# Performance work log

Hardware: AMD Instinct MI355X
Metric: run time of the kernel (lower is better)

## Reference

```python
import jax, jax.numpy as jnp
import numpy as np


def _deform_conv2d(x, offset, weight, stride=(1, 1), pad=(1, 1), dilation=(1, 1)):
    # x: [B,C,H,W]; offset: [B, 2*Goff*kh*kw, oh, ow]; weight: [OC, C//Gw, kh, kw]
    B, C, H, W = x.shape
    OC, Cg, kh, kw = weight.shape
    Gw = C // Cg
    K = kh * kw
    sh, sw = stride
    ph, pw = pad
    dh, dw = dilation
    oh = (H + 2 * ph - (dh * (kh - 1) + 1)) // sh + 1
    ow = (W + 2 * pw - (dw * (kw - 1) + 1)) // sw + 1
    Goff = offset.shape[1] // (2 * K)
    # torchvision layout: per offset group, per kernel tap k, (dy, dx)
    off = offset.reshape(B, Goff, K, 2, oh, ow)
    ki = jnp.arange(K) // kw  # kernel row per tap
    kj = jnp.arange(K) % kw   # kernel col per tap
    base_y = jnp.arange(oh) * sh - ph
    base_x = jnp.arange(ow) * sw - pw
    gy = (base_y[None, :] + (ki * dh)[:, None]).astype(x.dtype)  # [K, oh]
    gx = (base_x[None, :] + (kj * dw)[:, None]).astype(x.dtype)  # [K, ow]
    py = off[:, :, :, 0] + gy[None, None, :, :, None]  # [B,Goff,K,oh,ow]
    px = off[:, :, :, 1] + gx[None, None, :, None, :]
    cpg = C // Goff  # channels per offset group
    py = jnp.repeat(py, cpg, axis=1)  # [B,C,K,oh,ow]
    px = jnp.repeat(px, cpg, axis=1)
    xf = x.reshape(B, C, H * W)
    y0 = jnp.floor(py)
    x0 = jnp.floor(px)
    ty = py - y0
    tx = px - x0
    y0i = y0.astype(jnp.int32)
    x0i = x0.astype(jnp.int32)

    def gather(cy, cx):
        valid = (cy >= 0) & (cy < H) & (cx >= 0) & (cx < W)
        idx = jnp.clip(cy, 0, H - 1) * W + jnp.clip(cx, 0, W - 1)
        v = jnp.take_along_axis(xf, idx.reshape(B, C, -1), axis=2).reshape(idx.shape)
        return jnp.where(valid, v, jnp.zeros((), x.dtype))

    # bilinear sample, zero padding outside image (matches torchvision)
    v = (gather(y0i, x0i) * (1 - ty) * (1 - tx)
         + gather(y0i, x0i + 1) * (1 - ty) * tx
         + gather(y0i + 1, x0i) * ty * (1 - tx)
         + gather(y0i + 1, x0i + 1) * ty * tx)  # [B,C,K,oh,ow]
    v = v.reshape(B, Gw, Cg, K, oh, ow)
    wg = weight.reshape(Gw, OC // Gw, Cg, K)
    out = jnp.einsum('bgckhw,gock->bgohw', v, wg)
    return out.reshape(B, OC, oh, ow)


def setup_inputs() -> dict:
    key = jax.random.key(0)
    k1, k2, k3 = jax.random.split(key, 3)
    x = jax.random.normal(k1, (8, 64, 56, 56), dtype=jnp.float32)
    offset = jax.random.normal(k2, (8, 18, 56, 56), dtype=jnp.float32)
    weight = jax.random.normal(k3, (64, 64, 3, 3), dtype=jnp.float32) * 0.05
    return {"input": x, "offset": offset, "weight": weight}


def reference(input, offset, weight):
    return _deform_conv2d(input, offset, weight, stride=(1, 1), pad=(1, 1), dilation=(1, 1))
```

## Files before the change

### kernel.cpp

```cpp
#include <hip/hip_runtime.h>
#include <hip/hip_fp16.h>


typedef _Float16 f16x8 __attribute__((ext_vector_type(8)));
typedef float    f32x4 __attribute__((ext_vector_type(4)));

namespace {
constexpr int Bn = 8, Cn = 64, Hn = 56, Wn = 56;
constexpr int Kk = 9, OCn = 64;
constexpr int NPIX = 56 * 56;
constexpr int CK   = Cn * Kk;
constexpr int TP   = 32;
constexpr int TILES = NPIX / TP;
constexpr int XTILES = NPIX / 64;
constexpr int KSTEPS = CK / 32;
}

__device__ __forceinline__ __half2 u2h(unsigned u) {
    union { unsigned u; __half2 h; } x; x.u = u; return x.h;
}
__device__ __forceinline__ unsigned bcast_h(float f) {
    unsigned short hs = __half_as_ushort(__float2half(f));
    return (unsigned)hs * 0x10001u;
}
__device__ __forceinline__ void lds_barrier() {
    asm volatile("s_waitcnt lgkmcnt(0)" ::: "memory");
    __builtin_amdgcn_s_barrier();
}
__device__ __forceinline__ void gld16(uint4& d, const unsigned short* p) {
    asm volatile("global_load_dwordx4 %0, %1, off" : "=&v"(d) : "v"(p) : "memory");
}

__global__ __launch_bounds__(256) void prep_kernel(
    const float* __restrict__ x, const float* __restrict__ w,
    unsigned short* __restrict__ xh, unsigned short* __restrict__ wh2)
{
    const int tid = threadIdx.x;
    if (blockIdx.x >= 392) {
        const int i = (blockIdx.x - 392) * 256 + tid;
        if (i < OCn * CK) {
            const int j    = i & 7;
            const int lane = (i >> 3) & 63;
            const int rest = i >> 9;
            const int og   = rest / KSTEPS;
            const int oc   = og * 16 + (lane & 15);
            const int kglob = (rest % KSTEPS) * 32 + (lane >> 4) * 8 + j;
            const int tap = kglob >> 6;
            const int c   = kglob & 63;
            wh2[i] = __half_as_ushort(__float2half(w[oc * CK + c * Kk + tap]));
        }
        return;
    }
    __shared__ unsigned short lds[64][66];
    const int b  = blockIdx.x / XTILES;
    const int t0 = (blockIdx.x % XTILES) * 64;
    const float* xb = x + (size_t)b * Cn * NPIX;
    {
        const int hw0 = (tid & 15) * 4;
        #pragma unroll
        for (int i = 0; i < 4; ++i) {
            const int c = (tid >> 4) + i * 16;
            const float4 v = *(const float4*)(xb + (size_t)c * NPIX + t0 + hw0);
            lds[hw0 + 0][c] = __half_as_ushort(__float2half(v.x));
            lds[hw0 + 1][c] = __half_as_ushort(__float2half(v.y));
            lds[hw0 + 2][c] = __half_as_ushort(__float2half(v.z));
            lds[hw0 + 3][c] = __half_as_ushort(__float2half(v.w));
        }
    }
    __syncthreads();
    {
        const int co = (tid & 7) * 8;
        #pragma unroll
        for (int i = 0; i < 2; ++i) {
            const int hw = (tid >> 3) + i * 32;
            unsigned short tmp[8] __attribute__((aligned(16)));
            #pragma unroll
            for (int j = 0; j < 8; ++j) tmp[j] = lds[hw][co + j];
            *(uint4*)(xh + ((size_t)b * NPIX + t0 + hw) * Cn + co) = *(const uint4*)tmp;
        }
    }
}

__global__ __launch_bounds__(256, 3) void deform_fused(
    const unsigned short* __restrict__ xh, const float* __restrict__ off,
    const unsigned short* __restrict__ wh2, float* __restrict__ out)
{
    __shared__ uint4 smpw[Kk * TP];
    __shared__ int4  smpa[Kk * TP];
    __shared__ __align__(16) uint4 vbuf[3][8 * TP];

    const int tid = threadIdx.x;
    const int b  = blockIdx.x / TILES;
    const int p0 = (blockIdx.x % TILES) * TP;
    const unsigned short* xb = xh + (size_t)b * NPIX * Cn;
    const float* offb = off + (size_t)b * 18 * NPIX;

    for (int e = tid; e < Kk * TP; e += 256) {
        const int k  = e >> 5;
        const int px = e & 31;
        const int p  = p0 + px;
        const int oy = p / Wn, ox = p % Wn;
        const int ki = k / 3, kj = k % 3;
        const float offy = offb[(size_t)(2 * k)     * NPIX + p];
        const float offx = offb[(size_t)(2 * k + 1) * NPIX + p];
        const float py  = offy + (float)(oy - 1 + ki);
        const float pxv = offx + (float)(ox - 1 + kj);
        const float y0f = floorf(py), x0f = floorf(pxv);
        const float ty = py - y0f, tx = pxv - x0f;
        const int y0 = (int)y0f, x0 = (int)x0f;
        const int y1 = y0 + 1, x1 = x0 + 1;
        const bool vy0 = (y0 >= 0) & (y0 < Hn);
        const bool vy1 = (y1 >= 0) & (y1 < Hn);
        const bool vx0 = (x0 >= 0) & (x0 < Wn);
        const bool vx1 = (x1 >= 0) & (x1 < Wn);
        const int cy0 = min(max(y0, 0), Hn - 1);
        const int cy1 = min(max(y1, 0), Hn - 1);
        const int cx0 = min(max(x0, 0), Wn - 1);
        const int cx1 = min(max(x1, 0), Wn - 1);
        uint4 wq;
        wq.x = bcast_h((vy0 && vx0) ? (1.f - ty) * (1.f - tx) : 0.f);
        wq.y = bcast_h((vy0 && vx1) ? (1.f - ty) * tx         : 0.f);
        wq.z = bcast_h((vy1 && vx0) ? ty * (1.f - tx)         : 0.f);
        wq.w = bcast_h((vy1 && vx1) ? ty * tx                 : 0.f);
        int4 av;
        av.x = (cy0 * Wn + cx0) * Cn;
        av.y = (cy0 * Wn + cx1) * Cn;
        av.z = (cy1 * Wn + cx0) * Cn;
        av.w = (cy1 * Wn + cx1) * Cn;
        smpw[e] = wq;
        smpa[e] = av;
    }
    lds_barrier();
    asm volatile("s_waitcnt vmcnt(0)" ::: "memory");

    const int oct = tid & 7;
    const int gpx = (tid >> 3) & 31;
    const int co  = oct * 8;

    const int lane = tid & 63;
    const int og   = tid >> 6;
    const int hi   = lane >> 4;
    const int lr   = lane & 15;
    const uint4* ab = (const uint4*)wh2 + (size_t)og * KSTEPS * 64 + lane;

    uint4 s0[2], s1[2], s2[2], s3[2], wqr[2];
    uint4 aF[2][2];
    f32x4 acc0 = {0.f, 0.f, 0.f, 0.f};
    f32x4 acc1 = {0.f, 0.f, 0.f, 0.f};

    auto stageC = [&](int k) {
        const int sl = k & 1;
        const int m  = k * TP + gpx;
        const int4 av = smpa[m];
        wqr[sl] = smpw[m];
        gld16(s0[sl], xb + av.x + co);
        gld16(s1[sl], xb + av.y + co);
        gld16(s2[sl], xb + av.z + co);
        gld16(s3[sl], xb + av.w + co);
    };
    auto loadA = [&](int k) {
        const int sl = k & 1;
        gld16(aF[sl][0], (const unsigned short*)(ab + (k * 2 + 0) * 64));
        gld16(aF[sl][1], (const unsigned short*)(ab + (k * 2 + 1) * 64));
    };
    auto blend = [&](int k) {
        const int sl = k & 1;
        const __half2 w00 = u2h(wqr[sl].x), w01 = u2h(wqr[sl].y);
        const __half2 w10 = u2h(wqr[sl].z), w11 = u2h(wqr[sl].w);
        uint4 res;
        unsigned* rp = (unsigned*)&res;
        #pragma unroll
        for (int q = 0; q < 4; ++q) {
            __half2 a = __hmul2(w00, u2h(((const unsigned*)&s0[sl])[q]));
            a = __hfma2(w01, u2h(((const unsigned*)&s1[sl])[q]), a);
            a = __hfma2(w10, u2h(((const unsigned*)&s2[sl])[q]), a);
            a = __hfma2(w11, u2h(((const unsigned*)&s3[sl])[q]), a);
            rp[q] = *(const unsigned*)&a;
        }
        vbuf[k % 3][oct * TP + gpx] = res;
    };
    auto mfma = [&](int k) {
        const int sl = k % 3;
        #pragma unroll
        for (int kl = 0; kl < 2; ++kl) {
            const int octr = kl * 4 + hi;
            union { uint4 u; f16x8 h; } a, b0, b1;
            a.u  = aF[k & 1][kl];
            b0.u = vbuf[sl][octr * TP + lr];
            b1.u = vbuf[sl][octr * TP + 16 + lr];
            acc0 = __builtin_amdgcn_mfma_f32_16x16x32_f16(a.h, b0.h, acc0, 0, 0, 0);
            acc1 = __builtin_amdgcn_mfma_f32_16x16x32_f16(a.h, b1.h, acc1, 0, 0, 0);
        }
    };

    stageC(0); stageC(1);
    loadA(0);
    asm volatile("s_waitcnt vmcnt(6)" ::: "memory");
    __builtin_amdgcn_sched_barrier(0);
    blend(0);
    lds_barrier();

    #pragma unroll
    for (int k = 0; k < Kk; ++k) {
        if (k < Kk - 2) stageC(k + 2);
        if (k < Kk - 1) loadA(k + 1);
        if (k < Kk - 2)      asm volatile("s_waitcnt vmcnt(6)" ::: "memory");
        else if (k == Kk - 2) asm volatile("s_waitcnt vmcnt(2)" ::: "memory");
        else                  asm volatile("s_waitcnt vmcnt(0)" ::: "memory");
        __builtin_amdgcn_sched_barrier(0);
        if (k < Kk - 1) blend(k + 1);
        mfma(k);
        lds_barrier();
    }

    float* ob = out + ((size_t)b * OCn + og * 16 + hi * 4) * NPIX + p0 + lr;
    #pragma unroll
    for (int r = 0; r < 4; ++r) {
        ob[(size_t)r * NPIX]      = acc0[r];
        ob[(size_t)r * NPIX + 16] = acc1[r];
    }
}

extern "C" void kernel_launch(void* const* d_in, const int* in_sizes, int n_in,
                              void* d_out, int out_size, void* d_ws, size_t ws_size,
                              hipStream_t stream) {
    const float* x   = (const float*)d_in[0];
    const float* off = (const float*)d_in[1];
    const float* w   = (const float*)d_in[2];
    float* out = (float*)d_out;
    unsigned short* wh2 = (unsigned short*)d_ws;
    unsigned short* xh  = (unsigned short*)((char*)d_ws + 131072);

    hipLaunchKernelGGL(prep_kernel, dim3(392 + 144), dim3(256), 0, stream, x, w, xh, wh2);
    hipLaunchKernelGGL(deform_fused, dim3(Bn * TILES), dim3(256), 0, stream,
                       xh, off, wh2, out);
}
```

Before: 22.00 us.

## Halve block size so each wave computes two output-channel groups

The fused deform conv kernel now runs 128 threads per block instead of 256. Each thread gathers and blends two pixels per tap, and each wave issues MFMAs for two 16-channel output groups, reusing the same B fragments from LDS. This cuts the thread count and the LDS reads per MFMA and gives each wave more independent MFMA work. The cost is more registers per thread, deeper vmcnt waits and fewer waves per block to hide gather latency.

Result: no change. 22.18 us (+0.8%).

```diff
diff --git a/kernel.cpp b/kernel.cpp
--- a/kernel.cpp
+++ b/kernel.cpp
@@ -81,7 +81,7 @@
     }
 }
 
-__global__ __launch_bounds__(256, 3) void deform_fused(
+__global__ __launch_bounds__(128, 3) void deform_fused(
     const unsigned short* __restrict__ xh, const float* __restrict__ off,
     const unsigned short* __restrict__ wh2, float* __restrict__ out)
 {
@@ -95,7 +95,7 @@
     const unsigned short* xb = xh + (size_t)b * NPIX * Cn;
     const float* offb = off + (size_t)b * 18 * NPIX;
 
-    for (int e = tid; e < Kk * TP; e += 256) {
+    for (int e = tid; e < Kk * TP; e += 128) {
         const int k  = e >> 5;
         const int px = e & 31;
         const int p  = p0 + px;
@@ -133,69 +133,82 @@
     lds_barrier();
     asm volatile("s_waitcnt vmcnt(0)" ::: "memory");
 
-    const int oct = tid & 7;
-    const int gpx = (tid >> 3) & 31;
-    const int co  = oct * 8;
+    const int oct  = tid & 7;
+    const int gpx0 = (tid >> 3) & 15;
+    const int co   = oct * 8;
 
     const int lane = tid & 63;
-    const int og   = tid >> 6;
+    const int wv   = tid >> 6;
     const int hi   = lane >> 4;
     const int lr   = lane & 15;
-    const uint4* ab = (const uint4*)wh2 + (size_t)og * KSTEPS * 64 + lane;
-
-    uint4 s0[2], s1[2], s2[2], s3[2], wqr[2];
-    uint4 aF[2][2];
-    f32x4 acc0 = {0.f, 0.f, 0.f, 0.f};
-    f32x4 acc1 = {0.f, 0.f, 0.f, 0.f};
+    const uint4* ab0 = (const uint4*)wh2 + (size_t)(wv * 2 + 0) * KSTEPS * 64 + lane;
+    const uint4* ab1 = (const uint4*)wh2 + (size_t)(wv * 2 + 1) * KSTEPS * 64 + lane;
+
+    uint4 s0[2][2], s1[2][2], s2[2][2], s3[2][2], wqr[2][2];
+    uint4 aF[2][2][2];
+    f32x4 acc[2][2] = {{{0.f,0.f,0.f,0.f},{0.f,0.f,0.f,0.f}},
+                       {{0.f,0.f,0.f,0.f},{0.f,0.f,0.f,0.f}}};
 
     auto stageC = [&](int k) {
         const int sl = k & 1;
-        const int m  = k * TP + gpx;
-        const int4 av = smpa[m];
-        wqr[sl] = smpw[m];
-        gld16(s0[sl], xb + av.x + co);
-        gld16(s1[sl], xb + av.y + co);
-        gld16(s2[sl], xb + av.z + co);
-        gld16(s3[sl], xb + av.w + co);
+        #pragma unroll
+        for (int u = 0; u < 2; ++u) {
+            const int m  = k * TP + gpx0 + u * 16;
+            const int4 av = smpa[m];
+            wqr[sl][u] = smpw[m];
+            gld16(s0[sl][u], xb + av.x + co);
+            gld16(s1[sl][u], xb + av.y + co);
+            gld16(s2[sl][u], xb + av.z + co);
+            gld16(s3[sl][u], xb + av.w + co);
+        }
     };
     auto loadA = [&](int k) {
         const int sl = k & 1;
-        gld16(aF[sl][0], (const unsigned short*)(ab + (k * 2 + 0) * 64));
-        gld16(aF[sl][1], (const unsigned short*)(ab + (k * 2 + 1) * 64));
+        gld16(aF[sl][0][0], (const unsigned short*)(ab0 + (k * 2 + 0) * 64));
+        gld16(aF[sl][0][1], (const unsigned short*)(ab0 + (k * 2 + 1) * 64));
+        gld16(aF[sl][1][0], (const unsigned short*)(ab1 + (k * 2 + 0) * 64));
+        gld16(aF[sl][1][1], (const unsigned short*)(ab1 + (k * 2 + 1) * 64));
     };
     auto blend = [&](int k) {
         const int sl = k & 1;
-        const __half2 w00 = u2h(wqr[sl].x), w01 = u2h(wqr[sl].y);
-        const __half2 w10 = u2h(wqr[sl].z), w11 = u2h(wqr[sl].w);
-        uint4 res;
-        unsigned* rp = (unsigned*)&res;
-        #pragma unroll
-        for (int q = 0; q < 4; ++q) {
-            __half2 a = __hmul2(w00, u2h(((const unsigned*)&s0[sl])[q]));
-            a = __hfma2(w01, u2h(((const unsigned*)&s1[sl])[q]), a);
-            a = __hfma2(w10, u2h(((const unsigned*)&s2[sl])[q]), a);
-            a = __hfma2(w11, u2h(((const unsigned*)&s3[sl])[q]), a);
-            rp[q] = *(const unsigned*)&a;
-        }
-        vbuf[k % 3][oct * TP + gpx] = res;
+        #pragma unroll
+        for (int u = 0; u < 2; ++u) {
+            const __half2 w00 = u2h(wqr[sl][u].x), w01 = u2h(wqr[sl][u].y);
+            const __half2 w10 = u2h(wqr[sl][u].z), w11 = u2h(wqr[sl][u].w);
+            uint4 res;
+            unsigned* rp = (unsigned*)&res;
+            #pragma unroll
+            for (int q = 0; q < 4; ++q) {
+                __half2 a = __hmul2(w00, u2h(((const unsigned*)&s0[sl][u])[q]));
+                a = __hfma2(w01, u2h(((const unsigned*)&s1[sl][u])[q]), a);
+                a = __hfma2(w10, u2h(((const unsigned*)&s2[sl][u])[q]), a);
+                a = __hfma2(w11, u2h(((const unsigned*)&s3[sl][u])[q]), a);
+                rp[q] = *(const unsigned*)&a;
+            }
+            vbuf[k % 3][oct * TP + gpx0 + u * 16] = res;
+        }
     };
     auto mfma = [&](int k) {
         const int sl = k % 3;
         #pragma unroll
         for (int kl = 0; kl < 2; ++kl) {
             const int octr = kl * 4 + hi;
-            union { uint4 u; f16x8 h; } a, b0, b1;
-            a.u  = aF[k & 1][kl];
+            union { uint4 u; f16x8 h; } b0, b1;
             b0.u = vbuf[sl][octr * TP + lr];
             b1.u = vbuf[sl][octr * TP + 16 + lr];
-            acc0 = __builtin_amdgcn_mfma_f32_16x16x32_f16(a.h, b0.h, acc0, 0, 0, 0);
-            acc1 = __builtin_amdgcn_mfma_f32_16x16x32_f16(a.h, b1.h, acc1, 0, 0, 0);
+            #pragma unroll
+            for (int ogi = 0; ogi < 2; ++ogi) {
+                union { uint4 u; f16x8 h; } a;
+                a.u = aF[k & 1][ogi][kl];
+                acc[ogi][0] = __builtin_amdgcn_mfma_f32_16x16x32_f16(a.h, b0.h, acc[ogi][0], 0, 0, 0);
+                acc[ogi][1] = __builtin_amdgcn_mfma_f32_16x16x32_f16(a.h, b1.h, acc[ogi][1], 0, 0, 0);
+            }
         }
     };
 
     stageC(0); stageC(1);
     loadA(0);
-    asm volatile("s_waitcnt vmcnt(6)" ::: "memory");
+    asm volatile("s_waitcnt vmcnt(12)" ::: "memory");
     __builtin_amdgcn_sched_barrier(0);
     blend(0);
     lds_barrier();
@@ -204,20 +217,23 @@
     for (int k = 0; k < Kk; ++k) {
         if (k < Kk - 2) stageC(k + 2);
         if (k < Kk - 1) loadA(k + 1);
-        if (k < Kk - 2)      asm volatile("s_waitcnt vmcnt(6)" ::: "memory");
-        else if (k == Kk - 2) asm volatile("s_waitcnt vmcnt(2)" ::: "memory");
-        else                  asm volatile("s_waitcnt vmcnt(0)" ::: "memory");
+        if (k < Kk - 2)       asm volatile("s_waitcnt vmcnt(12)" ::: "memory");
+        else if (k == Kk - 2) asm volatile("s_waitcnt vmcnt(4)"  ::: "memory");
+        else                  asm volatile("s_waitcnt vmcnt(0)"  ::: "memory");
         __builtin_amdgcn_sched_barrier(0);
         if (k < Kk - 1) blend(k + 1);
         mfma(k);
         lds_barrier();
     }
 
-    float* ob = out + ((size_t)b * OCn + og * 16 + hi * 4) * NPIX + p0 + lr;
     #pragma unroll
-    for (int r = 0; r < 4; ++r) {
-        ob[(size_t)r * NPIX]      = acc0[r];
-        ob[(size_t)r * NPIX + 16] = acc1[r];
+    for (int ogi = 0; ogi < 2; ++ogi) {
+        float* ob = out + ((size_t)b * OCn + (wv * 2 + ogi) * 16 + hi * 4) * NPIX + p0 + lr;
+        #pragma unroll
+        for (int r = 0; r < 4; ++r) {
+            ob[(size_t)r * NPIX]      = acc[ogi][0][r];
+            ob[(size_t)r * NPIX + 16] = acc[ogi][1][r];
+        }
     }
 }
 
@@ -232,6 +248,6 @@
     unsigned short* xh  = (unsigned short*)((char*)d_ws + 131072);
 
     hipLaunchKernelGGL(prep_kernel, dim3(392 + 144), dim3(256), 0, stream, x, w, xh, wh2);
-    hipLaunchKernelGGL(deform_fused, dim3(Bn * TILES), dim3(256), 0, stream,
+    hipLaunchKernelGGL(deform_fused, dim3(Bn * TILES), dim3(128), 0, stream,
                        xh, off, wh2, out);
 }
```
